# Kernel optimization log

Hardware: AMD Instinct MI355X
Metric: run time of the kernel (lower is better)

## Reference

```python
import jax, jax.numpy as jnp
import numpy as np

B, T = 32, 64
INPUT_DIM, EMB, HA, HB, NUM_CLASS = 4894, 128, 128, 128, 1
D_IN = EMB + 1  # use_time=True appends scalar time feature


def gru_cell(x, h, Wih, Whh, bih, bhh):
    # torch nn.GRU cell semantics, gate order (r, z, n)
    gi = x @ Wih.T + bih
    gh = h @ Whh.T + bhh
    ir, iz, i_n = jnp.split(gi, 3, axis=-1)
    hr, hz, hn = jnp.split(gh, 3, axis=-1)
    r = jax.nn.sigmoid(ir + hr)
    z = jax.nn.sigmoid(iz + hz)
    n = jnp.tanh(i_n + r * hn)
    return (1.0 - z) * n + z * h


def setup_inputs():
    key = jax.random.key(0)
    ks = jax.random.split(key, 14)
    f32 = jnp.float32
    s = lambda k, sh, sc: (jax.random.normal(k, sh) * sc).astype(f32)
    return {
        "x": jax.random.uniform(ks[0], (B, T, INPUT_DIM), dtype=f32),
        "t": jax.random.uniform(ks[1], (B, T), dtype=f32),
        "lengths": jax.random.randint(ks[2], (B,), 1, T + 1),
        "W_emb": s(ks[3], (EMB, INPUT_DIM), 0.02),
        "Wih_a": s(ks[4], (3 * HA, D_IN), 0.05),
        "Whh_a": s(ks[5], (3 * HA, HA), 0.05),
        "bih_a": jnp.zeros((3 * HA,), f32),
        "bhh_a": jnp.zeros((3 * HA,), f32),
        "Wih_b": s(ks[6], (3 * HB, D_IN), 0.05),
        "Whh_b": s(ks[7], (3 * HB, HB), 0.05),
        "bih_b": jnp.zeros((3 * HB,), f32),
        "bhh_b": jnp.zeros((3 * HB,), f32),
        "w_alpha": s(ks[8], (1, HA), 0.1),
        "b_alpha": jnp.zeros((1,), f32),
        "W_beta": s(ks[9], (EMB, HB), 0.1),
        "b_beta": jnp.zeros((EMB,), f32),
        "W_out": s(ks[10], (NUM_CLASS, EMB), 0.1),
        "b_out": jnp.zeros((NUM_CLASS,), f32),
    }


def reference(x, t, lengths, W_emb, Wih_a, Whh_a, bih_a, bhh_a,
              Wih_b, Whh_b, bih_b, bhh_b, w_alpha, b_alpha,
              W_beta, b_beta, W_out, b_out):
    # embedding (dropout is identity in inference)
    emb = x @ W_emb.T                                   # [B,T,E]
    temb = jnp.concatenate([emb, t[..., None]], axis=-1)  # [B,T,E+1]

    # reversed-prefix tensor: R[b,i,k] = temb[b, i-k] for k<=i else 0
    i_idx = jnp.arange(T)[:, None]
    k_idx = jnp.arange(T)[None, :]
    src = i_idx - k_idx                                  # [T,T]
    valid = (src >= 0)
    src_c = jnp.clip(src, 0)
    vmask = valid[None, :, :, None].astype(emb.dtype)
    R = jnp.take(temb, src_c, axis=1) * vmask            # [B,T,T,D_IN]
    E_rev = jnp.take(emb, src_c, axis=1) * vmask         # [B,T,T,E]

    # run alpha/beta GRUs along the prefix axis k (causal, so zero padding
    # at k>i never affects the k<=i outputs that we keep)
    R_k = jnp.moveaxis(R, 2, 0)                          # [Tk,B,T,D_IN]
    h0a = jnp.zeros((B, T, HA), emb.dtype)
    h0b = jnp.zeros((B, T, HB), emb.dtype)

    def step(carry, xk):
        ha, hb = carry
        ha = gru_cell(xk, ha, Wih_a, Whh_a, bih_a, bhh_a)
        hb = gru_cell(xk, hb, Wih_b, Whh_b, bih_b, bhh_b)
        return (ha, hb), (ha, hb)

    _, (Ha, Hb) = jax.lax.scan(step, (h0a, h0b), R_k)
    Ha = jnp.moveaxis(Ha, 0, 2)                          # [B,T,Tk,HA]
    Hb = jnp.moveaxis(Hb, 0, 2)                          # [B,T,Tk,HB]

    # attention over the i+1 prefix positions
    scores = (Ha @ w_alpha.T + b_alpha)[..., 0]          # [B,T,Tk]
    scores = jnp.where(valid[None], scores, jnp.float32(-1e9))
    alpha = jax.nn.softmax(scores, axis=-1)
    beta = jnp.tanh(Hb @ W_beta.T + b_beta)              # [B,T,Tk,E]

    c = jnp.einsum('btk,btke,btke->bte', alpha, beta, E_rev)
    row_valid = (jnp.arange(T)[None, :] < lengths[:, None]).astype(c.dtype)
    c = c * row_valid[..., None]                         # zero where i >= lengths[b]

    logits = c @ W_out.T + b_out                         # [B,T,1]
    return logits[..., 0]
```

## Files before the change

kernel.cpp:

```cpp
#include <hip/hip_runtime.h>
#include <hip/hip_bf16.h>

#define DEVI __device__ __forceinline__

typedef __attribute__((ext_vector_type(8))) short short8;
typedef __attribute__((ext_vector_type(8))) unsigned short ushort8;
typedef __attribute__((ext_vector_type(4))) unsigned short ushort4v;
typedef __attribute__((ext_vector_type(4))) float f32x4;

static constexpr int TT = 64, KIN = 4894, KINP = 4896, E = 128;
static constexpr float L2E = 1.4426950408889634f;

DEVI unsigned short f2bf(float f) {
    union { float f; unsigned u; } v; v.f = f;
    unsigned r = v.u + 0x7fffu + ((v.u >> 16) & 1u);
    return (unsigned short)(r >> 16);
}
DEVI float sigm2(float x) { return __builtin_amdgcn_rcpf(1.f + __builtin_amdgcn_exp2f(-x)); }
DEVI float tanh2(float x) { return 1.f - 2.f * __builtin_amdgcn_rcpf(__builtin_amdgcn_exp2f(x + x) + 1.f); }

__global__ void prep_kernel(const float* __restrict__ Wemb,
                            const float* __restrict__ Wih_a, const float* __restrict__ Wih_b,
                            const float* __restrict__ Whh_a, const float* __restrict__ Whh_b,
                            const float* __restrict__ Wbeta,
                            unsigned short* __restrict__ wembbf, unsigned short* __restrict__ wihbf,
                            unsigned short* __restrict__ whhbf, unsigned short* __restrict__ wbetabf) {
    int job = blockIdx.x * blockDim.x + threadIdx.x;
    const int JWE = 128 * 612, JWIH = 768 * 16, JWHH = 768 * 16, JWB = 128 * 16;
    if (job < JWE) {
        int row = job / 612, c8 = (job % 612) * 8;
        ushort8 v;
        #pragma unroll
        for (int jj = 0; jj < 8; ++jj) { int c = c8 + jj; v[jj] = (c < KIN) ? f2bf(Wemb[(long)row * KIN + c]) : (unsigned short)0; }
        *(ushort8*)(wembbf + (long)row * KINP + c8) = v;
        return;
    }
    job -= JWE;
    if (job < JWIH) {
        int g = job / 16, c8 = (job % 16) * 8;
        const float* src = (g < 384) ? (Wih_a + (long)g * 129) : (Wih_b + (long)(g - 384) * 129);
        ushort8 v;
        #pragma unroll
        for (int jj = 0; jj < 8; ++jj) v[jj] = f2bf(src[c8 + jj] * L2E);
        *(ushort8*)(wihbf + (long)g * 128 + c8) = v;
        return;
    }
    job -= JWIH;
    if (job < JWHH) {
        int g = job / 16, c8 = (job % 16) * 8;
        const float* src = (g < 384) ? (Whh_a + (long)g * 128) : (Whh_b + (long)(g - 384) * 128);
        ushort8 v;
        #pragma unroll
        for (int jj = 0; jj < 8; ++jj) v[jj] = f2bf(src[c8 + jj] * L2E);
        *(ushort8*)(whhbf + (long)g * 128 + c8) = v;
        return;
    }
    job -= JWHH;
    if (job < JWB) {
        int e = job / 16, c8 = (job % 16) * 8;
        ushort8 v;
        #pragma unroll
        for (int jj = 0; jj < 8; ++jj) v[jj] = f2bf(Wbeta[(long)e * 128 + c8 + jj] * L2E);
        *(ushort8*)(wbetabf + (long)e * 128 + c8) = v;
    }
}

__global__ __launch_bounds__(256) void emb_gemm(const float* __restrict__ x,
                                                const unsigned short* __restrict__ wembbf,
                                                float* __restrict__ pout) {
    const int ks = blockIdx.x & 3, m0 = (blockIdx.x >> 2) * 16;
    const int w = threadIdx.x >> 6, l = threadIdx.x & 63, lr = l & 15, lo = l >> 4;
    const int n0 = (2 * w) * 16 + lr, n1 = (2 * w + 1) * 16 + lr;
    const float* xrow = x + (long)(m0 + lr) * KIN;
    const int k0 = ks * 1216;
    const int nfull = 38;
    f32x4 acc0 = {0, 0, 0, 0}, acc1 = {0, 0, 0, 0};
    #pragma unroll 2
    for (int kt = 0; kt < nfull; ++kt) {
        int k = k0 + kt * 32 + lo * 8;
        float2 x0 = *(const float2*)(xrow + k);
        float2 x1 = *(const float2*)(xrow + k + 2);
        float2 x2 = *(const float2*)(xrow + k + 4);
        float2 x3 = *(const float2*)(xrow + k + 6);
        short8 a;
        a[0] = (short)f2bf(x0.x); a[1] = (short)f2bf(x0.y);
        a[2] = (short)f2bf(x1.x); a[3] = (short)f2bf(x1.y);
        a[4] = (short)f2bf(x2.x); a[5] = (short)f2bf(x2.y);
        a[6] = (short)f2bf(x3.x); a[7] = (short)f2bf(x3.y);
        short8 b0 = *(const short8*)(wembbf + (long)n0 * KINP + k);
        short8 b1 = *(const short8*)(wembbf + (long)n1 * KINP + k);
        acc0 = __builtin_amdgcn_mfma_f32_16x16x32_bf16(a, b0, acc0, 0, 0, 0);
        acc1 = __builtin_amdgcn_mfma_f32_16x16x32_bf16(a, b1, acc1, 0, 0, 0);
    }
    if (ks == 3) {
        int k = 4864 + lo * 8;
        short8 a;
        #pragma unroll
        for (int jj = 0; jj < 8; ++jj) { int c = k + jj; a[jj] = (c < KIN) ? (short)f2bf(xrow[c]) : (short)0; }
        short8 b0 = *(const short8*)(wembbf + (long)n0 * KINP + k);
        short8 b1 = *(const short8*)(wembbf + (long)n1 * KINP + k);
        acc0 = __builtin_amdgcn_mfma_f32_16x16x32_bf16(a, b0, acc0, 0, 0, 0);
        acc1 = __builtin_amdgcn_mfma_f32_16x16x32_bf16(a, b1, acc1, 0, 0, 0);
    }
    float* pbase = pout + (long)ks * 2048 * E;
    #pragma unroll
    for (int r = 0; r < 4; ++r) {
        int m = m0 + lo * 4 + r;
        pbase[(long)m * E + n0] = acc0[r];
        pbase[(long)m * E + n1] = acc1[r];
    }
}

__global__ __launch_bounds__(256) void emb_reduce(const float* __restrict__ pout,
                                                  float* __restrict__ emb, unsigned short* __restrict__ embbf) {
    const long idx = (long)blockIdx.x * 256 + threadIdx.x;
    const long base = idx * 4;
    f32x4 s = *(const f32x4*)(pout + base);
    #pragma unroll
    for (int ks = 1; ks < 4; ++ks) {
        f32x4 v = *(const f32x4*)(pout + (long)ks * 2048 * E + base);
        s[0] += v[0]; s[1] += v[1]; s[2] += v[2]; s[3] += v[3];
    }
    *(f32x4*)(emb + base) = s;
    ushort4v h;
    #pragma unroll
    for (int jj = 0; jj < 4; ++jj) h[jj] = f2bf(s[jj]);
    *(ushort4v*)(embbf + base) = h;
}

__global__ __launch_bounds__(256) void gi_gemm(const unsigned short* __restrict__ embbf,
                                               const unsigned short* __restrict__ wihbf,
                                               const float* __restrict__ Wih_a, const float* __restrict__ Wih_b,
                                               const float* __restrict__ t,
                                               const float* __restrict__ bih_a, const float* __restrict__ bih_b,
                                               const float* __restrict__ bhh_a, const float* __restrict__ bhh_b,
                                               float* __restrict__ Gi3) {
    const int m0 = blockIdx.x * 16;
    const int w = threadIdx.x >> 6, l = threadIdx.x & 63, lr = l & 15, lo = l >> 4;
    f32x4 acc[12];
    #pragma unroll
    for (int nl = 0; nl < 12; ++nl) acc[nl] = (f32x4){0, 0, 0, 0};
    #pragma unroll
    for (int kt = 0; kt < 4; ++kt) {
        int k = kt * 32 + lo * 8;
        short8 a0 = *(const short8*)(embbf + (long)(m0 + lr) * E + k);
        #pragma unroll
        for (int nl = 0; nl < 12; ++nl) {
            int n = (w * 12 + nl) * 16 + lr;
            short8 bf = *(const short8*)(wihbf + (long)n * 128 + k);
            acc[nl] = __builtin_amdgcn_mfma_f32_16x16x32_bf16(a0, bf, acc[nl], 0, 0, 0);
        }
    }
    #pragma unroll
    for (int nl = 0; nl < 12; ++nl) {
        int n = (w * 12 + nl) * 16 + lr;
        int gru = (n >= 384) ? 1 : 0;
        int nn = n - gru * 384;
        int gt = nn >> 7, u = nn & 127;
        float bias = (gru ? bih_b[nn] : bih_a[nn]);
        if (gt < 2) bias += (gru ? bhh_b[nn] : bhh_a[nn]);
        float cw = (n < 384) ? Wih_a[(long)n * 129 + 128] : Wih_b[(long)(n - 384) * 129 + 128];
        #pragma unroll
        for (int r = 0; r < 4; ++r) {
            int tok = m0 + lo * 4 + r;
            Gi3[((long)(tok * 2 + gru) * 128 + u) * 4 + gt] = acc[nl][r] + (bias + t[tok] * cw) * L2E;
        }
    }
}

__global__ __launch_bounds__(512) __attribute__((amdgpu_waves_per_eu(2, 2)))
void retain_rec(const unsigned short* __restrict__ whhbf, const unsigned short* __restrict__ wbetabf,
                const float* __restrict__ Gi3, const float* __restrict__ emb,
                const float* __restrict__ bhh_a, const float* __restrict__ bhh_b,
                const float* __restrict__ w_alpha, const float* __restrict__ b_alpha,
                const float* __restrict__ b_beta, const float* __restrict__ Wout,
                float* __restrict__ p_g, float* __restrict__ d_g) {
    const int tid = threadIdx.x;
    const int w = tid >> 6, l = tid & 63, lr = l & 15, lo = l >> 4;
    const int i = blockIdx.x >> 2, q = (blockIdx.x >> 1) & 1, g = blockIdx.x & 1;
    const int u = w * 16 + lr;

    __shared__ __align__(16) unsigned short Hbf[2][16][128];
    __shared__ float red[2][8][16];
    __shared__ float pd_s[16][66];

    for (int idx = tid; idx < 2 * 16 * 128; idx += 512) (&Hbf[0][0][0])[idx] = 0;

    short8 Wf[3][4];
    #pragma unroll
    for (int gt = 0; gt < 3; ++gt)
        #pragma unroll
        for (int kt = 0; kt < 4; ++kt)
            Wf[gt][kt] = *(const short8*)(whhbf + (long)(g * 384 + gt * 128 + u) * 128 + kt * 32 + lo * 8);

    short8 Xf[4];
    float bbetL = 0.f, wo = 0.f;
    if (g) {
        #pragma unroll
        for (int kt = 0; kt < 4; ++kt)
            Xf[kt] = *(const short8*)(wbetabf + (long)u * 128 + kt * 32 + lo * 8);
        bbetL = b_beta[u] * L2E;
        wo = Wout[u];
    } else {
        #pragma unroll
        for (int kt = 0; kt < 4; ++kt) {
            short8 z;
            #pragma unroll
            for (int jj = 0; jj < 8; ++jj) z[jj] = 0;
            Xf[kt] = z;
        }
    }

    const float bhnL = (g ? bhh_b : bhh_a)[256 + u] * L2E;
    const float waL = g ? 0.f : w_alpha[u] * L2E;
    const float balL = b_alpha[0] * L2E;

    float h_old[4] = {0, 0, 0, 0};

    f32x4 giv[4];
    #pragma unroll
    for (int r = 0; r < 4; ++r) {
        int tok = (q * 16 + lo * 4 + r) * 64 + i;
        giv[r] = *(const f32x4*)(Gi3 + ((long)(tok * 2 + g) * 128 + u) * 4);
    }
    float ev[4] = {0, 0, 0, 0};
    if (g) {
        #pragma unroll
        for (int r = 0; r < 4; ++r) {
            int tok = (q * 16 + lo * 4 + r) * 64 + i;
            ev[r] = emb[(long)tok * E + u];
        }
    }

    __syncthreads();

    const int iend = i + 1 + g;
    for (int n = 0; n <= iend; ++n) {
        const int rb = n & 1, wb = rb ^ 1;
        const bool do_gate = (n <= i);
        const bool do_post = (n >= 1) && (n <= i + 1);

        f32x4 givn[4];
        float evn[4];
        const bool ld_gi = (n < i);
        const bool ld_ev = g && (n <= i);
        if (ld_gi) {
            const int jn = i - n - 1;
            #pragma unroll
            for (int r = 0; r < 4; ++r) {
                int tok = (q * 16 + lo * 4 + r) * 64 + jn;
                givn[r] = *(const f32x4*)(Gi3 + ((long)(tok * 2 + g) * 128 + u) * 4);
            }
        }
        if (ld_ev) {
            const int j2n = i - n;
            #pragma unroll
            for (int r = 0; r < 4; ++r) {
                int tok = (q * 16 + lo * 4 + r) * 64 + j2n;
                evn[r] = emb[(long)tok * E + u];
            }
        }

        if (w == 0 && l < 16) {
            if (!g) {
                if (do_post) {
                    float s = balL;
                    #pragma unroll
                    for (int ww = 0; ww < 8; ++ww) s += red[wb][ww][l];
                    pd_s[l][n - 1] = __builtin_amdgcn_exp2f(s);
                }
            } else {
                if (n >= 2) {
                    float d = 0.f;
                    #pragma unroll
                    for (int ww = 0; ww < 8; ++ww) d += red[wb][ww][l];
                    pd_s[l][n - 2] = d;
                }
            }
        }

        short8 Af[4];
        if (do_gate || (g && do_post)) {
            #pragma unroll
            for (int kt = 0; kt < 4; ++kt) {
                int sw = (kt * 32 + lo * 8) ^ ((lr & 7) * 8);
                Af[kt] = *(const short8*)(&Hbf[rb][lr][sw]);
            }
        }

        f32x4 gh0 = {0, 0, 0, 0}, gh1 = {0, 0, 0, 0}, gh2 = {bhnL, bhnL, bhnL, bhnL};
        f32x4 xacc = {0, 0, 0, 0};
        if (do_gate) {
            #pragma unroll
            for (int kt = 0; kt < 4; ++kt) {
                gh0 = __builtin_amdgcn_mfma_f32_16x16x32_bf16(Af[kt], Wf[0][kt], gh0, 0, 0, 0);
                gh1 = __builtin_amdgcn_mfma_f32_16x16x32_bf16(Af[kt], Wf[1][kt], gh1, 0, 0, 0);
                gh2 = __builtin_amdgcn_mfma_f32_16x16x32_bf16(Af[kt], Wf[2][kt], gh2, 0, 0, 0);
            }
        }
        if (g && do_post) {
            #pragma unroll
            for (int kt = 0; kt < 4; ++kt)
                xacc = __builtin_amdgcn_mfma_f32_16x16x32_bf16(Af[kt], Xf[kt], xacc, 0, 0, 0);
            float dp[4];
            #pragma unroll
            for (int r = 0; r < 4; ++r) dp[r] = tanh2(xacc[r] + bbetL) * ev[r] * wo;
            #pragma unroll
            for (int r = 0; r < 4; ++r) {
                dp[r] += __shfl_xor(dp[r], 1);
                dp[r] += __shfl_xor(dp[r], 2);
                dp[r] += __shfl_xor(dp[r], 4);
                dp[r] += __shfl_xor(dp[r], 8);
            }
            if (lr == 0) {
                #pragma unroll
                for (int r = 0; r < 4; ++r) red[rb][w][lo * 4 + r] = dp[r];
            }
        }

        if (do_gate) {
            float sp[4];
            #pragma unroll
            for (int r = 0; r < 4; ++r) {
                f32x4 gv = giv[r];
                float rr = sigm2(gv[0] + gh0[r]);
                float zz = sigm2(gv[1] + gh1[r]);
                float nn = tanh2(gv[2] + rr * gh2[r]);
                float h = nn + zz * (h_old[r] - nn);
                h_old[r] = h;
                int c = lo * 4 + r;
                Hbf[wb][c][u ^ ((c & 7) * 8)] = f2bf(h);
                sp[r] = h * waL;
            }
            if (!g) {
                #pragma unroll
                for (int r = 0; r < 4; ++r) {
                    sp[r] += __shfl_xor(sp[r], 1);
                    sp[r] += __shfl_xor(sp[r], 2);
                    sp[r] += __shfl_xor(sp[r], 4);
                    sp[r] += __shfl_xor(sp[r], 8);
                }
                if (lr == 0) {
                    #pragma unroll
                    for (int r = 0; r < 4; ++r) red[rb][w][lo * 4 + r] = sp[r];
                }
            }
        }

        if (ld_gi) {
            #pragma unroll
            for (int r = 0; r < 4; ++r) giv[r] = givn[r];
        }
        if (ld_ev) {
            #pragma unroll
            for (int r = 0; r < 4; ++r) ev[r] = evn[r];
        }

        __syncthreads();
    }

    float* dst = g ? d_g : p_g;
    for (int idx = tid; idx < 16 * 64; idx += 512) {
        int c = idx >> 6, kk = idx & 63;
        if (kk <= i) {
            long row = (long)(q * 16 + c) * 64 + i;
            dst[row * 64 + kk] = pd_s[c][kk];
        }
    }
}

__global__ __launch_bounds__(512) void reduce_out(const float* __restrict__ p_g, const float* __restrict__ d_g,
                                                  const int* __restrict__ lengths, const float* __restrict__ b_out,
                                                  float* __restrict__ out) {
    const int w = threadIdx.x >> 6, l = threadIdx.x & 63;
    const int row = blockIdx.x * 8 + w;
    const int b = row >> 6, i = row & 63;
    float p = (l <= i) ? p_g[(long)row * 64 + l] : 0.f;
    float d = (l <= i) ? d_g[(long)row * 64 + l] : 0.f;
    float pd = p * d;
    #pragma unroll
    for (int off = 1; off < 64; off <<= 1) {
        p += __shfl_xor(p, off);
        pd += __shfl_xor(pd, off);
    }
    if (l == 0) {
        float val = (i < lengths[b]) ? pd / p + b_out[0] : b_out[0];
        out[row] = val;
    }
}

extern "C" void kernel_launch(void* const* d_in, const int* in_sizes, int n_in,
                              void* d_out, int out_size, void* d_ws, size_t ws_size,
                              hipStream_t stream) {
    (void)in_sizes; (void)n_in; (void)out_size; (void)ws_size;
    const float* x       = (const float*)d_in[0];
    const float* t       = (const float*)d_in[1];
    const int*   len     = (const int*)d_in[2];
    const float* Wemb    = (const float*)d_in[3];
    const float* Wih_a   = (const float*)d_in[4];
    const float* Whh_a   = (const float*)d_in[5];
    const float* bih_a   = (const float*)d_in[6];
    const float* bhh_a   = (const float*)d_in[7];
    const float* Wih_b   = (const float*)d_in[8];
    const float* Whh_b   = (const float*)d_in[9];
    const float* bih_b   = (const float*)d_in[10];
    const float* bhh_b   = (const float*)d_in[11];
    const float* w_alpha = (const float*)d_in[12];
    const float* b_alpha = (const float*)d_in[13];
    const float* W_beta  = (const float*)d_in[14];
    const float* b_beta  = (const float*)d_in[15];
    const float* W_out   = (const float*)d_in[16];
    const float* b_out   = (const float*)d_in[17];

    char* ws = (char*)d_ws;
    float*          emb     = (float*)(ws + 0);
    unsigned short* embbf   = (unsigned short*)(ws + 1048576);
    float*          Gi3     = (float*)(ws + 1572864);
    unsigned short* wembbf  = (unsigned short*)(ws + 9961472);
    unsigned short* wihbf   = (unsigned short*)(ws + 11214848);
    unsigned short* whhbf   = (unsigned short*)(ws + 11411456);
    unsigned short* wbetabf = (unsigned short*)(ws + 11608064);
    float*          p_g     = (float*)(ws + 11640832);
    float*          d_g     = (float*)(ws + 12165120);
    float*          pout    = (float*)(ws + 12689408);

    const int jobs = 128 * 612 + 768 * 16 + 768 * 16 + 128 * 16;
    prep_kernel<<<(jobs + 255) / 256, 256, 0, stream>>>(Wemb, Wih_a, Wih_b, Whh_a, Whh_b, W_beta,
                                                        wembbf, wihbf, whhbf, wbetabf);
    emb_gemm<<<512, 256, 0, stream>>>(x, wembbf, pout);
    emb_reduce<<<256, 256, 0, stream>>>(pout, emb, embbf);
    gi_gemm<<<128, 256, 0, stream>>>(embbf, wihbf, Wih_a, Wih_b, t, bih_a, bih_b, bhh_a, bhh_b, Gi3);
    retain_rec<<<256, 512, 0, stream>>>(whhbf, wbetabf, Gi3, emb, bhh_a, bhh_b,
                                        w_alpha, b_alpha, b_beta, W_out, p_g, d_g);
    reduce_out<<<256, 512, 0, stream>>>(p_g, d_g, len, b_out, (float*)d_out);
}
```

Baseline: 160.3 us.

## Drop weight prep kernel, convert weights inline, restructure alpha score via MFMA

Removes the separate bf16 weight-conversion kernel: each GEMM and the recurrence kernel now load fp32 weights and convert them to bf16 in registers. In the recurrence, the alpha-score reduction now runs through the MFMA path, with w_alpha used as a broadcast B operand, instead of shuffle reductions plus a cross-wave LDS sum. Gi/emb pointers are stepped incrementally, hidden states are packed with v_cvt_pk_bf16_f32, and __syncthreads is replaced by a bare lgkmcnt wait plus s_barrier. The trade is one fewer launch and less workspace traffic against repeated fp32 weight loads and conversions inside emb_gemm, and a barrier that may not wait for outstanding global memory operations.

New measurement: 180.3 us. 1.12x slower.

```diff
diff --git a/kernel.cpp b/kernel.cpp
--- a/kernel.cpp
+++ b/kernel.cpp
@@ -4,11 +4,10 @@
 #define DEVI __device__ __forceinline__
 
 typedef __attribute__((ext_vector_type(8))) short short8;
-typedef __attribute__((ext_vector_type(8))) unsigned short ushort8;
 typedef __attribute__((ext_vector_type(4))) unsigned short ushort4v;
 typedef __attribute__((ext_vector_type(4))) float f32x4;
 
-static constexpr int TT = 64, KIN = 4894, KINP = 4896, E = 128;
+static constexpr int TT = 64, KIN = 4894, E = 128;
 static constexpr float L2E = 1.4426950408889634f;
 
 DEVI unsigned short f2bf(float f) {
@@ -19,86 +18,59 @@
 DEVI float sigm2(float x) { return __builtin_amdgcn_rcpf(1.f + __builtin_amdgcn_exp2f(-x)); }
 DEVI float tanh2(float x) { return 1.f - 2.f * __builtin_amdgcn_rcpf(__builtin_amdgcn_exp2f(x + x) + 1.f); }
 
-__global__ void prep_kernel(const float* __restrict__ Wemb,
-                            const float* __restrict__ Wih_a, const float* __restrict__ Wih_b,
-                            const float* __restrict__ Whh_a, const float* __restrict__ Whh_b,
-                            const float* __restrict__ Wbeta,
-                            unsigned short* __restrict__ wembbf, unsigned short* __restrict__ wihbf,
-                            unsigned short* __restrict__ whhbf, unsigned short* __restrict__ wbetabf) {
-    int job = blockIdx.x * blockDim.x + threadIdx.x;
-    const int JWE = 128 * 612, JWIH = 768 * 16, JWHH = 768 * 16, JWB = 128 * 16;
-    if (job < JWE) {
-        int row = job / 612, c8 = (job % 612) * 8;
-        ushort8 v;
-        #pragma unroll
-        for (int jj = 0; jj < 8; ++jj) { int c = c8 + jj; v[jj] = (c < KIN) ? f2bf(Wemb[(long)row * KIN + c]) : (unsigned short)0; }
-        *(ushort8*)(wembbf + (long)row * KINP + c8) = v;
-        return;
-    }
-    job -= JWE;
-    if (job < JWIH) {
-        int g = job / 16, c8 = (job % 16) * 8;
-        const float* src = (g < 384) ? (Wih_a + (long)g * 129) : (Wih_b + (long)(g - 384) * 129);
-        ushort8 v;
-        #pragma unroll
-        for (int jj = 0; jj < 8; ++jj) v[jj] = f2bf(src[c8 + jj] * L2E);
-        *(ushort8*)(wihbf + (long)g * 128 + c8) = v;
-        return;
-    }
-    job -= JWIH;
-    if (job < JWHH) {
-        int g = job / 16, c8 = (job % 16) * 8;
-        const float* src = (g < 384) ? (Whh_a + (long)g * 128) : (Whh_b + (long)(g - 384) * 128);
-        ushort8 v;
-        #pragma unroll
-        for (int jj = 0; jj < 8; ++jj) v[jj] = f2bf(src[c8 + jj] * L2E);
-        *(ushort8*)(whhbf + (long)g * 128 + c8) = v;
-        return;
-    }
-    job -= JWHH;
-    if (job < JWB) {
-        int e = job / 16, c8 = (job % 16) * 8;
-        ushort8 v;
-        #pragma unroll
-        for (int jj = 0; jj < 8; ++jj) v[jj] = f2bf(Wbeta[(long)e * 128 + c8 + jj] * L2E);
-        *(ushort8*)(wbetabf + (long)e * 128 + c8) = v;
-    }
+DEVI void bar_lds() {
+    asm volatile("s_waitcnt lgkmcnt(0)" ::: "memory");
+    __builtin_amdgcn_s_barrier();
+}
+
+DEVI short8 cvt8(const float* __restrict__ p, float s) {
+    float2 v0 = *(const float2*)p, v1 = *(const float2*)(p + 2);
+    float2 v2 = *(const float2*)(p + 4), v3 = *(const float2*)(p + 6);
+    short8 r;
+    r[0] = (short)f2bf(v0.x * s); r[1] = (short)f2bf(v0.y * s);
+    r[2] = (short)f2bf(v1.x * s); r[3] = (short)f2bf(v1.y * s);
+    r[4] = (short)f2bf(v2.x * s); r[5] = (short)f2bf(v2.y * s);
+    r[6] = (short)f2bf(v3.x * s); r[7] = (short)f2bf(v3.y * s);
+    return r;
+}
+DEVI short8 cvt8s(const float* __restrict__ p, float s) {
+    short8 r;
+    #pragma unroll
+    for (int jj = 0; jj < 8; ++jj) r[jj] = (short)f2bf(p[jj] * s);
+    return r;
 }
 
 __global__ __launch_bounds__(256) void emb_gemm(const float* __restrict__ x,
-                                                const unsigned short* __restrict__ wembbf,
+                                                const float* __restrict__ Wemb,
                                                 float* __restrict__ pout) {
     const int ks = blockIdx.x & 3, m0 = (blockIdx.x >> 2) * 16;
     const int w = threadIdx.x >> 6, l = threadIdx.x & 63, lr = l & 15, lo = l >> 4;
     const int n0 = (2 * w) * 16 + lr, n1 = (2 * w + 1) * 16 + lr;
     const float* xrow = x + (long)(m0 + lr) * KIN;
+    const float* w0 = Wemb + (long)n0 * KIN;
+    const float* w1 = Wemb + (long)n1 * KIN;
     const int k0 = ks * 1216;
-    const int nfull = 38;
     f32x4 acc0 = {0, 0, 0, 0}, acc1 = {0, 0, 0, 0};
     #pragma unroll 2
-    for (int kt = 0; kt < nfull; ++kt) {
+    for (int kt = 0; kt < 38; ++kt) {
         int k = k0 + kt * 32 + lo * 8;
-        float2 x0 = *(const float2*)(xrow + k);
-        float2 x1 = *(const float2*)(xrow + k + 2);
-        float2 x2 = *(const float2*)(xrow + k + 4);
-        float2 x3 = *(const float2*)(xrow + k + 6);
-        short8 a;
-        a[0] = (short)f2bf(x0.x); a[1] = (short)f2bf(x0.y);
-        a[2] = (short)f2bf(x1.x); a[3] = (short)f2bf(x1.y);
-        a[4] = (short)f2bf(x2.x); a[5] = (short)f2bf(x2.y);
-        a[6] = (short)f2bf(x3.x); a[7] = (short)f2bf(x3.y);
-        short8 b0 = *(const short8*)(wembbf + (long)n0 * KINP + k);
-        short8 b1 = *(const short8*)(wembbf + (long)n1 * KINP + k);
+        short8 a  = cvt8(xrow + k, 1.f);
+        short8 b0 = cvt8(w0 + k, 1.f);
+        short8 b1 = cvt8(w1 + k, 1.f);
         acc0 = __builtin_amdgcn_mfma_f32_16x16x32_bf16(a, b0, acc0, 0, 0, 0);
         acc1 = __builtin_amdgcn_mfma_f32_16x16x32_bf16(a, b1, acc1, 0, 0, 0);
     }
     if (ks == 3) {
         int k = 4864 + lo * 8;
-        short8 a;
+        short8 a, b0, b1;
         #pragma unroll
-        for (int jj = 0; jj < 8; ++jj) { int c = k + jj; a[jj] = (c < KIN) ? (short)f2bf(xrow[c]) : (short)0; }
-        short8 b0 = *(const short8*)(wembbf + (long)n0 * KINP + k);
-        short8 b1 = *(const short8*)(wembbf + (long)n1 * KINP + k);
+        for (int jj = 0; jj < 8; ++jj) {
+            int c = k + jj;
+            bool ok = (c < KIN);
+            a[jj]  = ok ? (short)f2bf(xrow[c]) : (short)0;
+            b0[jj] = ok ? (short)f2bf(w0[c]) : (short)0;
+            b1[jj] = ok ? (short)f2bf(w1[c]) : (short)0;
+        }
         acc0 = __builtin_amdgcn_mfma_f32_16x16x32_bf16(a, b0, acc0, 0, 0, 0);
         acc1 = __builtin_amdgcn_mfma_f32_16x16x32_bf16(a, b1, acc1, 0, 0, 0);
     }
@@ -129,7 +101,6 @@
 }
 
 __global__ __launch_bounds__(256) void gi_gemm(const unsigned short* __restrict__ embbf,
-                                               const unsigned short* __restrict__ wihbf,
                                                const float* __restrict__ Wih_a, const float* __restrict__ Wih_b,
                                                const float* __restrict__ t,
                                                const float* __restrict__ bih_a, const float* __restrict__ bih_b,
@@ -147,7 +118,8 @@
         #pragma unroll
         for (int nl = 0; nl < 12; ++nl) {
             int n = (w * 12 + nl) * 16 + lr;
-            short8 bf = *(const short8*)(wihbf + (long)n * 128 + k);
+            const float* src = ((n < 384) ? (Wih_a + (long)n * 129) : (Wih_b + (long)(n - 384) * 129)) + k;
+            short8 bf = cvt8s(src, L2E);
             acc[nl] = __builtin_amdgcn_mfma_f32_16x16x32_bf16(a0, bf, acc[nl], 0, 0, 0);
         }
     }
@@ -169,7 +141,8 @@
 }
 
 __global__ __launch_bounds__(512) __attribute__((amdgpu_waves_per_eu(2, 2)))
-void retain_rec(const unsigned short* __restrict__ whhbf, const unsigned short* __restrict__ wbetabf,
+void retain_rec(const float* __restrict__ Whh_a, const float* __restrict__ Whh_b,
+                const float* __restrict__ Wbeta,
                 const float* __restrict__ Gi3, const float* __restrict__ emb,
                 const float* __restrict__ bhh_a, const float* __restrict__ bhh_b,
                 const float* __restrict__ w_alpha, const float* __restrict__ b_alpha,
@@ -186,51 +159,39 @@
 
     for (int idx = tid; idx < 2 * 16 * 128; idx += 512) (&Hbf[0][0][0])[idx] = 0;
 
+    const float* WhhG = g ? Whh_b : Whh_a;
     short8 Wf[3][4];
     #pragma unroll
     for (int gt = 0; gt < 3; ++gt)
         #pragma unroll
         for (int kt = 0; kt < 4; ++kt)
-            Wf[gt][kt] = *(const short8*)(whhbf + (long)(g * 384 + gt * 128 + u) * 128 + kt * 32 + lo * 8);
+            Wf[gt][kt] = cvt8(WhhG + (long)(gt * 128 + u) * 128 + kt * 32 + lo * 8, L2E);
 
     short8 Xf[4];
-    float bbetL = 0.f, wo = 0.f;
-    if (g) {
-        #pragma unroll
-        for (int kt = 0; kt < 4; ++kt)
-            Xf[kt] = *(const short8*)(wbetabf + (long)u * 128 + kt * 32 + lo * 8);
-        bbetL = b_beta[u] * L2E;
-        wo = Wout[u];
-    } else {
-        #pragma unroll
-        for (int kt = 0; kt < 4; ++kt) {
-            short8 z;
-            #pragma unroll
-            for (int jj = 0; jj < 8; ++jj) z[jj] = 0;
-            Xf[kt] = z;
-        }
-    }
+    #pragma unroll
+    for (int kt = 0; kt < 4; ++kt)
+        Xf[kt] = g ? cvt8(Wbeta + (long)u * 128 + kt * 32 + lo * 8, L2E)
+                   : cvt8(w_alpha + kt * 32 + lo * 8, L2E);
 
     const float bhnL = (g ? bhh_b : bhh_a)[256 + u] * L2E;
-    const float waL = g ? 0.f : w_alpha[u] * L2E;
+    const float bbetL = g ? b_beta[u] * L2E : 0.f;
+    const float wo = g ? Wout[u] : 0.f;
     const float balL = b_alpha[0] * L2E;
 
     float h_old[4] = {0, 0, 0, 0};
 
-    f32x4 giv[4];
+    const f32x4* gp[4];
+    const float* ep[4];
     #pragma unroll
     for (int r = 0; r < 4; ++r) {
         int tok = (q * 16 + lo * 4 + r) * 64 + i;
-        giv[r] = *(const f32x4*)(Gi3 + ((long)(tok * 2 + g) * 128 + u) * 4);
-    }
+        gp[r] = (const f32x4*)Gi3 + ((long)(tok * 2 + g) * 128 + u);
+        ep[r] = emb + (long)tok * E + u;
+    }
+    f32x4 giv[4];
+    #pragma unroll
+    for (int r = 0; r < 4; ++r) giv[r] = *gp[r];
     float ev[4] = {0, 0, 0, 0};
-    if (g) {
-        #pragma unroll
-        for (int r = 0; r < 4; ++r) {
-            int tok = (q * 16 + lo * 4 + r) * 64 + i;
-            ev[r] = emb[(long)tok * E + u];
-        }
-    }
 
     __syncthreads();
 
@@ -239,48 +200,29 @@
         const int rb = n & 1, wb = rb ^ 1;
         const bool do_gate = (n <= i);
         const bool do_post = (n >= 1) && (n <= i + 1);
+        const bool ld_gi = (n < i);
+        const bool ld_ev = g && (n <= i);
 
         f32x4 givn[4];
         float evn[4];
-        const bool ld_gi = (n < i);
-        const bool ld_ev = g && (n <= i);
         if (ld_gi) {
-            const int jn = i - n - 1;
-            #pragma unroll
-            for (int r = 0; r < 4; ++r) {
-                int tok = (q * 16 + lo * 4 + r) * 64 + jn;
-                givn[r] = *(const f32x4*)(Gi3 + ((long)(tok * 2 + g) * 128 + u) * 4);
-            }
+            #pragma unroll
+            for (int r = 0; r < 4; ++r) { gp[r] -= 256; givn[r] = *gp[r]; }
         }
         if (ld_ev) {
-            const int j2n = i - n;
-            #pragma unroll
-            for (int r = 0; r < 4; ++r) {
-                int tok = (q * 16 + lo * 4 + r) * 64 + j2n;
-                evn[r] = emb[(long)tok * E + u];
-            }
-        }
-
-        if (w == 0 && l < 16) {
-            if (!g) {
-                if (do_post) {
-                    float s = balL;
-                    #pragma unroll
-                    for (int ww = 0; ww < 8; ++ww) s += red[wb][ww][l];
-                    pd_s[l][n - 1] = __builtin_amdgcn_exp2f(s);
-                }
-            } else {
-                if (n >= 2) {
-                    float d = 0.f;
-                    #pragma unroll
-                    for (int ww = 0; ww < 8; ++ww) d += red[wb][ww][l];
-                    pd_s[l][n - 2] = d;
-                }
-            }
+            #pragma unroll
+            for (int r = 0; r < 4; ++r) { evn[r] = *ep[r]; ep[r] -= E; }
+        }
+
+        if (g && w == 0 && l < 16 && n >= 2) {
+            float d = 0.f;
+            #pragma unroll
+            for (int ww = 0; ww < 8; ++ww) d += red[wb][ww][l];
+            pd_s[l][n - 2] = d;
         }
 
         short8 Af[4];
-        if (do_gate || (g && do_post)) {
+        if (do_gate || do_post) {
             #pragma unroll
             for (int kt = 0; kt < 4; ++kt) {
                 int sw = (kt * 32 + lo * 8) ^ ((lr & 7) * 8);
@@ -289,7 +231,6 @@
         }
 
         f32x4 gh0 = {0, 0, 0, 0}, gh1 = {0, 0, 0, 0}, gh2 = {bhnL, bhnL, bhnL, bhnL};
-        f32x4 xacc = {0, 0, 0, 0};
         if (do_gate) {
             #pragma unroll
             for (int kt = 0; kt < 4; ++kt) {
@@ -298,53 +239,56 @@
                 gh2 = __builtin_amdgcn_mfma_f32_16x16x32_bf16(Af[kt], Wf[2][kt], gh2, 0, 0, 0);
             }
         }
-        if (g && do_post) {
+
+        if (do_post) {
+            f32x4 xacc = {0, 0, 0, 0};
             #pragma unroll
             for (int kt = 0; kt < 4; ++kt)
                 xacc = __builtin_amdgcn_mfma_f32_16x16x32_bf16(Af[kt], Xf[kt], xacc, 0, 0, 0);
-            float dp[4];
-            #pragma unroll
-            for (int r = 0; r < 4; ++r) dp[r] = tanh2(xacc[r] + bbetL) * ev[r] * wo;
-            #pragma unroll
-            for (int r = 0; r < 4; ++r) {
-                dp[r] += __shfl_xor(dp[r], 1);
-                dp[r] += __shfl_xor(dp[r], 2);
-                dp[r] += __shfl_xor(dp[r], 4);
-                dp[r] += __shfl_xor(dp[r], 8);
+            if (!g) {
+                if (w == 0 && lr == 0) {
+                    #pragma unroll
+                    for (int r = 0; r < 4; ++r)
+                        pd_s[lo * 4 + r][n - 1] = __builtin_amdgcn_exp2f(xacc[r] + balL);
+                }
+            } else {
+                float dp[4];
+                #pragma unroll
+                for (int r = 0; r < 4; ++r) dp[r] = tanh2(xacc[r] + bbetL) * ev[r] * wo;
+                #pragma unroll
+                for (int r = 0; r < 4; ++r) {
+                    dp[r] += __shfl_xor(dp[r], 1);
+                    dp[r] += __shfl_xor(dp[r], 2);
+                    dp[r] += __shfl_xor(dp[r], 4);
+                    dp[r] += __shfl_xor(dp[r], 8);
+                }
+                if (lr == 0) {
+                    #pragma unroll
+                    for (int r = 0; r < 4; ++r) red[rb][w][lo * 4 + r] = dp[r];
+                }
             }
-            if (lr == 0) {
-                #pragma unroll
-                for (int r = 0; r < 4; ++r) red[rb][w][lo * 4 + r] = dp[r];
-            }
         }
 
         if (do_gate) {
-            float sp[4];
+            float hn[4];
             #pragma unroll
             for (int r = 0; r < 4; ++r) {
                 f32x4 gv = giv[r];
                 float rr = sigm2(gv[0] + gh0[r]);
                 float zz = sigm2(gv[1] + gh1[r]);
-                float nn = tanh2(gv[2] + rr * gh2[r]);
-                float h = nn + zz * (h_old[r] - nn);
+                float nnv = tanh2(gv[2] + rr * gh2[r]);
+                float h = nnv + zz * (h_old[r] - nnv);
                 h_old[r] = h;
-                int c = lo * 4 + r;
-                Hbf[wb][c][u ^ ((c & 7) * 8)] = f2bf(h);
-                sp[r] = h * waL;
+                hn[r] = h;
             }
-            if (!g) {
-                #pragma unroll
-                for (int r = 0; r < 4; ++r) {
-                    sp[r] += __shfl_xor(sp[r], 1);
-                    sp[r] += __shfl_xor(sp[r], 2);
-                    sp[r] += __shfl_xor(sp[r], 4);
-                    sp[r] += __shfl_xor(sp[r], 8);
-                }
-                if (lr == 0) {
-                    #pragma unroll
-                    for (int r = 0; r < 4; ++r) red[rb][w][lo * 4 + r] = sp[r];
-                }
-            }
+            unsigned pk01, pk23;
+            asm("v_cvt_pk_bf16_f32 %0, %1, %2" : "=v"(pk01) : "v"(hn[0]), "v"(hn[1]));
+            asm("v_cvt_pk_bf16_f32 %0, %1, %2" : "=v"(pk23) : "v"(hn[2]), "v"(hn[3]));
+            const int c0 = lo * 4;
+            Hbf[wb][c0 + 0][u ^ (((c0 + 0) & 7) * 8)] = (unsigned short)pk01;
+            Hbf[wb][c0 + 1][u ^ (((c0 + 1) & 7) * 8)] = (unsigned short)(pk01 >> 16);
+            Hbf[wb][c0 + 2][u ^ (((c0 + 2) & 7) * 8)] = (unsigned short)pk23;
+            Hbf[wb][c0 + 3][u ^ (((c0 + 3) & 7) * 8)] = (unsigned short)(pk23 >> 16);
         }
 
         if (ld_gi) {
@@ -356,7 +300,7 @@
             for (int r = 0; r < 4; ++r) ev[r] = evn[r];
         }
 
-        __syncthreads();
+        bar_lds();
     }
 
     float* dst = g ? d_g : p_g;
@@ -413,24 +357,17 @@
     const float* b_out   = (const float*)d_in[17];
 
     char* ws = (char*)d_ws;
-    float*          emb     = (float*)(ws + 0);
-    unsigned short* embbf   = (unsigned short*)(ws + 1048576);
-    float*          Gi3     = (float*)(ws + 1572864);
-    unsigned short* wembbf  = (unsigned short*)(ws + 9961472);
-    unsigned short* wihbf   = (unsigned short*)(ws + 11214848);
-    unsigned short* whhbf   = (unsigned short*)(ws + 11411456);
-    unsigned short* wbetabf = (unsigned short*)(ws + 11608064);
-    float*          p_g     = (float*)(ws + 11640832);
-    float*          d_g     = (float*)(ws + 12165120);
-    float*          pout    = (float*)(ws + 12689408);
-
-    const int jobs = 128 * 612 + 768 * 16 + 768 * 16 + 128 * 16;
-    prep_kernel<<<(jobs + 255) / 256, 256, 0, stream>>>(Wemb, Wih_a, Wih_b, Whh_a, Whh_b, W_beta,
-                                                        wembbf, wihbf, whhbf, wbetabf);
-    emb_gemm<<<512, 256, 0, stream>>>(x, wembbf, pout);
+    float*          emb   = (float*)(ws + 0);
+    unsigned short* embbf = (unsigned short*)(ws + 1048576);
+    float*          Gi3   = (float*)(ws + 1572864);
+    float*          p_g   = (float*)(ws + 9961472);
+    float*          d_g   = (float*)(ws + 10485760);
+    float*          pout  = (float*)(ws + 11010048);
+
+    emb_gemm<<<512, 256, 0, stream>>>(x, Wemb, pout);
     emb_reduce<<<256, 256, 0, stream>>>(pout, emb, embbf);
-    gi_gemm<<<128, 256, 0, stream>>>(embbf, wihbf, Wih_a, Wih_b, t, bih_a, bih_b, bhh_a, bhh_b, Gi3);
-    retain_rec<<<256, 512, 0, stream>>>(whhbf, wbetabf, Gi3, emb, bhh_a, bhh_b,
+    gi_gemm<<<128, 256, 0, stream>>>(embbf, Wih_a, Wih_b, t, bih_a, bih_b, bhh_a, bhh_b, Gi3);
+    retain_rec<<<256, 512, 0, stream>>>(Whh_a, Whh_b, W_beta, Gi3, emb, bhh_a, bhh_b,
                                         w_alpha, b_alpha, b_beta, W_out, p_g, d_g);
     reduce_out<<<256, 512, 0, stream>>>(p_g, d_g, len, b_out, (float*)d_out);
 }
```
